# Performance work log

Hardware: AMD Instinct MI355X
Metric: run time of the kernel (lower is better)

The kernel has to match this reference:

```python
import jax, jax.numpy as jnp
import numpy as np

CLUSTER_DIM = 64
SHRINKAGE = True
EPS = 1e-8


def setup_inputs() -> dict:
    key = jax.random.key(0)
    x = jax.random.normal(key, (256, CLUSTER_DIM, 4096), dtype=jnp.float32)
    return {"x": x}


def _mat_shrinkage(C, n):
    # Rao-Blackwellized Ledoit-Wolf shrinkage toward scaled identity.
    p = CLUSTER_DIM
    I = jnp.eye(p, dtype=C.dtype)[None, :, :]
    trace = jnp.trace(C, axis1=-2, axis2=-1)[:, None, None]          # [B,1,1]
    F_hat = trace / p * I
    second_trace = jnp.einsum('bij,bji->b', C, C)[:, None, None]      # tr(C @ C)
    numerator = (n - 2) / n * second_trace + trace ** 2
    denominator = (n + 2) * (second_trace - trace ** 2 / p)
    rho = jnp.minimum(numerator / denominator, 1.0)
    return rho * F_hat + (1.0 - rho) * C


def reference(x):
    B, C, M = x.shape  # C == CLUSTER_DIM
    x_mu = jnp.mean(x, axis=2, keepdims=True)
    x_cnt = x - x_mu                                                  # [B,C,M]
    cov = jnp.einsum('bcm,bdm->bcd', x_cnt, x_cnt) / M                # [B,C,C]
    if SHRINKAGE:
        cov = _mat_shrinkage(cov, n=M)
    L, Q = jnp.linalg.eigh(cov)                                       # L:[B,C] Q:[B,C,C]
    L = jnp.maximum(L, EPS)
    # S_hat = Q @ diag(L^-1/2) @ Q^T, fused as scaled columns of Q
    S_hat = jnp.einsum('bik,bk,bjk->bij', Q, jax.lax.rsqrt(L), Q)     # [B,C,C]
    Z = jnp.einsum('bij,bjm->bim', S_hat, x_cnt)                      # [B,C,M]
    return Z
```

## Files before the change

### kernel.cpp

```cpp
#include <hip/hip_runtime.h>
#include <hip/hip_bf16.h>

#define BB 256
#define P 64
#define MM 4096
#define MC 128
#define MT 256

using bf16x8 = __attribute__((ext_vector_type(8))) short;
using f32x16 = __attribute__((ext_vector_type(16))) float;
using f32x4  = __attribute__((ext_vector_type(4))) float;
using u32x4  = __attribute__((ext_vector_type(4))) unsigned;
using u32x2  = __attribute__((ext_vector_type(2))) unsigned;

__device__ inline f32x16 MF(bf16x8 a, bf16x8 b, f32x16 c) {
    return __builtin_amdgcn_mfma_f32_32x32x16_bf16(a, b, c, 0, 0, 0);
}
__device__ inline unsigned cvtpk(float lo, float hi) {
    unsigned u;
    asm("v_cvt_pk_bf16_f32 %0, %1, %2" : "=v"(u) : "v"(lo), "v"(hi));
    return u;
}

template<bool XPK>
__global__ __launch_bounds__(256)
void covpart_kernel(const float* __restrict__ x, float* __restrict__ s2p,
                    float* __restrict__ s1p, unsigned* __restrict__ xpk, int nsplit)
{
    __shared__ __align__(16) unsigned char smem[34816];

    const int b = blockIdx.x, sp = blockIdx.y;
    const int t = threadIdx.x;
    const int w = t >> 6, l = t & 63;
    const int lr = l & 31, lh = l >> 5;
    const int mlen = MM / nsplit;
    const float* xb = x + (size_t)b * (P * MM) + (size_t)sp * mlen;
    unsigned* xpb = XPK ? (xpk + (size_t)b * (32 * MM) + (size_t)sp * mlen) : nullptr;

    f32x16 acc0 = {0,0,0,0,0,0,0,0,0,0,0,0,0,0,0,0};
    f32x16 acc1 = {0,0,0,0,0,0,0,0,0,0,0,0,0,0,0,0};
    f32x16 acc2 = {0,0,0,0,0,0,0,0,0,0,0,0,0,0,0,0};
    float s1e[4] = {0.f,0.f,0.f,0.f};
    float s1o[4] = {0.f,0.f,0.f,0.f};

    const int kbase = lh * 16;
    const int nch = mlen / MC;

    f32x4 ve[4], vo[4];
    #pragma unroll
    for (int j = 0; j < 4; ++j) {
        int slot = t + 256 * j;
        int dp = slot >> 5, c = (slot & 31) << 2;
        const float* p = xb + (size_t)(2 * dp) * MM + c;
        ve[j] = *reinterpret_cast<const f32x4*>(p);
        vo[j] = *reinterpret_cast<const f32x4*>(p + MM);
    }

    for (int ch = 0; ch < nch; ++ch) {
        char* buf = (char*)smem + (ch & 1) * 17408;
        #pragma unroll
        for (int j = 0; j < 4; ++j) {
            int slot = t + 256 * j;
            int dp = slot >> 5, c4 = slot & 31;
            float e0 = ve[j].x, e1 = ve[j].y, e2 = ve[j].z, e3 = ve[j].w;
            float o0 = vo[j].x, o1 = vo[j].y, o2 = vo[j].z, o3 = vo[j].w;
            s1e[j] += (e0 + e1) + (e2 + e3);
            s1o[j] += (o0 + o1) + (o2 + o3);
            u32x2 he, ho;
            he.x = cvtpk(e0, e1); he.y = cvtpk(e2, e3);
            ho.x = cvtpk(o0, o1); ho.y = cvtpk(o2, o3);
            char* dst = buf + (2 * dp) * 272 + c4 * 8;
            *reinterpret_cast<u32x2*>(dst) = he;
            *reinterpret_cast<u32x2*>(dst + 272) = ho;
            if (XPK) {
                u32x4 pd;
                pd.x = cvtpk(e0, o0); pd.y = cvtpk(e1, o1);
                pd.z = cvtpk(e2, o2); pd.w = cvtpk(e3, o3);
                *reinterpret_cast<u32x4*>(xpb + (size_t)dp * MM + ch * MC + c4 * 4) = pd;
            }
        }
        if (ch + 1 < nch) {
            const int m0 = (ch + 1) * MC;
            #pragma unroll
            for (int j = 0; j < 4; ++j) {
                int slot = t + 256 * j;
                int dp = slot >> 5, c = (slot & 31) << 2;
                const float* p = xb + (size_t)(2 * dp) * MM + m0 + c;
                ve[j] = *reinterpret_cast<const f32x4*>(p);
                vo[j] = *reinterpret_cast<const f32x4*>(p + MM);
            }
        }
        __syncthreads();
        #pragma unroll
        for (int kk = 0; kk < 2; ++kk) {
            const int kb = (2 * w + kk) * 32 + kbase;
            bf16x8 f0 = *(const bf16x8*)(buf + lr * 272 + kb);
            bf16x8 f1 = *(const bf16x8*)(buf + (32 + lr) * 272 + kb);
            acc0 = MF(f0, f0, acc0);
            acc1 = MF(f0, f1, acc1);
            acc2 = MF(f1, f1, acc2);
        }
    }

    float (*T)[32][33] = reinterpret_cast<float (*)[32][33]>(smem);
    float* s2b = s2p + ((size_t)sp * BB + b) * (P * P);

#define REDUCE_PASS(ACC, STORE)                                       \
    {                                                                 \
        __syncthreads();                                              \
        _Pragma("unroll")                                             \
        for (int n = 0; n < 16; ++n) {                                \
            int row = (n & 3) + 8 * (n >> 2) + 4 * lh;                \
            T[w][row][lr] = ACC[n];                                   \
        }                                                             \
        __syncthreads();                                              \
        _Pragma("unroll")                                             \
        for (int q = 0; q < 4; ++q) {                                 \
            int idx = t + 256 * q;                                    \
            int r = idx >> 5, c = idx & 31;                           \
            float s = T[0][r][c] + T[1][r][c] + T[2][r][c] + T[3][r][c]; \
            STORE                                                     \
        }                                                             \
    }

    REDUCE_PASS(acc0, s2b[r * 64 + c] = s;)
    REDUCE_PASS(acc1, s2b[r * 64 + 32 + c] = s; s2b[(32 + c) * 64 + r] = s;)
    REDUCE_PASS(acc2, s2b[(32 + r) * 64 + 32 + c] = s;)
#undef REDUCE_PASS

    #pragma unroll
    for (int m = 16; m >= 1; m >>= 1) {
        #pragma unroll
        for (int j = 0; j < 4; ++j) {
            s1e[j] += __shfl_xor(s1e[j], m);
            s1o[j] += __shfl_xor(s1o[j], m);
        }
    }
    if ((t & 31) == 0) {
        float* s1b = s1p + ((size_t)sp * BB + b) * P;
        int g = t >> 5;
        #pragma unroll
        for (int j = 0; j < 4; ++j) {
            int r0 = 2 * (g + 8 * j);
            s1b[r0]     = s1e[j];
            s1b[r0 + 1] = s1o[j];
        }
    }
}

typedef float (*Mat68)[68];

__device__ inline void mm64f(Mat68 D, Mat68 A, Mat68 Bm, int t, float alpha, float beta)
{
    __syncthreads();
    const int r0 = (t >> 4) * 4, c0 = (t & 15) * 4;
    float acc[4][4];
    #pragma unroll
    for (int i = 0; i < 4; ++i)
        #pragma unroll
        for (int j = 0; j < 4; ++j) acc[i][j] = 0.f;
    #pragma unroll 4
    for (int k = 0; k < P; ++k) {
        float av[4], bv[4];
        *reinterpret_cast<float4*>(av) = *reinterpret_cast<const float4*>(&A[k][r0]);
        *reinterpret_cast<float4*>(bv) = *reinterpret_cast<const float4*>(&Bm[k][c0]);
        #pragma unroll
        for (int i = 0; i < 4; ++i)
            #pragma unroll
            for (int j = 0; j < 4; ++j) acc[i][j] += av[i] * bv[j];
    }
    __syncthreads();
    #pragma unroll
    for (int i = 0; i < 4; ++i)
        #pragma unroll
        for (int j = 0; j < 4; ++j)
            D[r0 + i][c0 + j] = alpha * acc[i][j] + ((r0 + i) == (c0 + j) ? beta : 0.f);
}

__global__ __launch_bounds__(256)
void whiten_kernel(const float* __restrict__ s2p, const float* __restrict__ s1p,
                   unsigned* __restrict__ sbb, float* __restrict__ tvec, int nsplit)
{
    __shared__ __align__(16) float B0[P][68], B1[P][68], B2[P][68], B3[P][68], B4[P][68];
    __shared__ float mus[P];
    __shared__ float red[2][4];
    const int b = blockIdx.x, t = threadIdx.x;

    if (t < P) {
        float s = 0.f;
        for (int sp = 0; sp < nsplit; ++sp) s += s1p[((size_t)sp * BB + b) * P + t];
        mus[t] = s * (1.0f / MM);
    }
    __syncthreads();

    float tr_part = 0.f, s2_part = 0.f;
    #pragma unroll
    for (int j = 0; j < 16; ++j) {
        int f = t + 256 * j;
        int i = f >> 6, jc = f & 63;
        float sum = 0.f;
        for (int sp = 0; sp < nsplit; ++sp)
            sum += s2p[((size_t)sp * BB + b) * (P * P) + f];
        float v = sum * (1.0f / MM) - mus[i] * mus[jc];
        B0[i][jc] = v;
        s2_part += v * v;
        if (i == jc) tr_part += v;
    }
    #pragma unroll
    for (int off = 32; off > 0; off >>= 1) {
        tr_part += __shfl_down(tr_part, off);
        s2_part += __shfl_down(s2_part, off);
    }
    if ((t & 63) == 0) { red[0][t >> 6] = tr_part; red[1][t >> 6] = s2_part; }
    __syncthreads();
    const float trace = red[0][0] + red[0][1] + red[0][2] + red[0][3];
    const float sum2  = red[1][0] + red[1][1] + red[1][2] + red[1][3];

    const float nf = (float)MM;
    const float num = (nf - 2.0f) / nf * sum2 + trace * trace;
    const float den = (nf + 2.0f) * (sum2 - trace * trace / (float)P);
    const float rho = (den > 0.f) ? fminf(num / den, 1.0f) : 1.0f;
    const float lam = trace * (1.0f / P);
    const float inv_s = 1.0f / lam;

    #pragma unroll
    for (int j = 0; j < 16; ++j) {
        int f = t + 256 * j;
        int i = f >> 6, jc = f & 63;
        float v = B0[i][jc];
        float sv = ((1.0f - rho) * v + ((i == jc) ? rho * lam : 0.f)) * inv_s;
        B0[i][jc] = sv;
        B2[i][jc] = ((i == jc) ? 1.5f : 0.f) - 0.5f * sv;
    }

    mm64f(B1, B0, B2, t, 1.f, 0.f);
    Mat68 Yc = B1, Zc = B2, Tc = B0, U = B3, V = B4;
    {
        mm64f(Tc, Zc, Yc, t, -0.5f, 1.5f);
        mm64f(U,  Yc, Tc, t, 1.f, 0.f);
        mm64f(V,  Tc, Zc, t, 1.f, 0.f);
        Mat68 tmp = Yc; Yc = U; U = tmp;
        tmp = Zc; Zc = V; V = tmp;
    }
    mm64f(Tc, Zc, Yc, t, -0.5f, 1.5f);
    mm64f(U,  Tc, Zc, t, 1.f, 0.f);
    __syncthreads();

    const float sc = rsqrtf(lam);
    unsigned* sb = sbb + (size_t)b * (P * P / 2);
    #pragma unroll
    for (int j = 0; j < 8; ++j) {
        int slot = t + 256 * j;
        int dp = slot >> 6, row = slot & 63;
        sb[slot] = cvtpk(U[row][2 * dp] * sc, U[row][2 * dp + 1] * sc);
    }
    if (t < P) {
        float tv = 0.f;
        #pragma unroll
        for (int d = 0; d < P; ++d) tv += U[t][d] * mus[d];
        tvec[b * P + t] = tv * sc;
    }
}

__global__ __launch_bounds__(256)
void apply_kernel_x(const unsigned* __restrict__ xpk, const unsigned* __restrict__ sbb,
                    const float* __restrict__ tvec, float* __restrict__ out)
{
    __shared__ unsigned Spk[32][68];
    __shared__ unsigned Xpk[32][260];
    __shared__ float tvs[P];
    const int mt = blockIdx.x, b = blockIdx.y;
    const int t = threadIdx.x;
    const int w = t >> 6, l = t & 63;
    const int lr = l & 31, lh = l >> 5;

    const unsigned* sb = sbb + (size_t)b * (P * P / 2);
    #pragma unroll
    for (int j = 0; j < 8; ++j) {
        int slot = t + 256 * j;
        Spk[slot >> 6][slot & 63] = sb[slot];
    }
    if (t < P) tvs[t] = tvec[b * P + t];

    const unsigned* xb = xpk + (size_t)b * (32 * MM) + mt * MT;
    #pragma unroll
    for (int j = 0; j < 8; ++j) {
        int slot = t + 256 * j;
        int dp = slot >> 6, m0 = (slot & 63) * 4;
        u32x4 pk = *reinterpret_cast<const u32x4*>(xb + (size_t)dp * MM + m0);
        *reinterpret_cast<u32x4*>(&Xpk[dp][m0]) = pk;
    }
    __syncthreads();

    union U8 { unsigned u[4]; bf16x8 v; };
    bf16x8 sa0[4], sa1[4];
    #pragma unroll
    for (int ks = 0; ks < 4; ++ks) {
        const int dpb = ks * 8 + lh * 4;
        U8 x0, x1;
        #pragma unroll
        for (int q = 0; q < 4; ++q) {
            x0.u[q] = Spk[dpb + q][lr];
            x1.u[q] = Spk[dpb + q][32 + lr];
        }
        sa0[ks] = x0.v;
        sa1[ks] = x1.v;
    }

    f32x16 acc00 = {0,0,0,0,0,0,0,0,0,0,0,0,0,0,0,0};
    f32x16 acc01 = {0,0,0,0,0,0,0,0,0,0,0,0,0,0,0,0};
    f32x16 acc10 = {0,0,0,0,0,0,0,0,0,0,0,0,0,0,0,0};
    f32x16 acc11 = {0,0,0,0,0,0,0,0,0,0,0,0,0,0,0,0};

    const int cq0 = (2 * w) * 32 + lr, cq1 = cq0 + 32;
    #pragma unroll
    for (int ks = 0; ks < 4; ++ks) {
        const int dpb = ks * 8 + lh * 4;
        U8 b0, b1;
        #pragma unroll
        for (int q = 0; q < 4; ++q) {
            b0.u[q] = Xpk[dpb + q][cq0];
            b1.u[q] = Xpk[dpb + q][cq1];
        }
        acc00 = MF(sa0[ks], b0.v, acc00);
        acc01 = MF(sa0[ks], b1.v, acc01);
        acc10 = MF(sa1[ks], b0.v, acc10);
        acc11 = MF(sa1[ks], b1.v, acc11);
    }

    float* ob = out + (size_t)b * (P * MM) + mt * MT;
#define STORE_TILE(ACC, RT, CQ)                                          \
    {                                                                    \
        _Pragma("unroll")                                                \
        for (int n = 0; n < 16; ++n) {                                   \
            int row = (RT) * 32 + (n & 3) + 8 * (n >> 2) + 4 * lh;       \
            __builtin_nontemporal_store(ACC[n] - tvs[row],               \
                                        ob + (size_t)row * MM + (CQ));   \
        }                                                                \
    }
    STORE_TILE(acc00, 0, cq0)
    STORE_TILE(acc01, 0, cq1)
    STORE_TILE(acc10, 1, cq0)
    STORE_TILE(acc11, 1, cq1)
#undef STORE_TILE
}

__global__ __launch_bounds__(256)
void apply_kernel(const float* __restrict__ x, const unsigned* __restrict__ sbb,
                  const float* __restrict__ tvec, float* __restrict__ out)
{
    __shared__ unsigned Spk[32][68];
    __shared__ unsigned Xpk[32][260];
    __shared__ float tvs[P];
    const int mt = blockIdx.x, b = blockIdx.y;
    const int t = threadIdx.x;
    const int w = t >> 6, l = t & 63;
    const int lr = l & 31, lh = l >> 5;

    const unsigned* sb = sbb + (size_t)b * (P * P / 2);
    #pragma unroll
    for (int j = 0; j < 8; ++j) {
        int slot = t + 256 * j;
        Spk[slot >> 6][slot & 63] = sb[slot];
    }
    if (t < P) tvs[t] = tvec[b * P + t];

    const float* xb = x + (size_t)b * (P * MM) + mt * MT;
    #pragma unroll
    for (int j = 0; j < 8; ++j) {
        int slot = t + 256 * j;
        int dp = slot >> 6, m0 = (slot & 63) * 4;
        const float* xr = xb + (size_t)(2 * dp) * MM + m0;
        f32x4 a = *reinterpret_cast<const f32x4*>(xr);
        f32x4 c = *reinterpret_cast<const f32x4*>(xr + MM);
        uint4 pk = make_uint4(cvtpk(a.x, c.x), cvtpk(a.y, c.y),
                              cvtpk(a.z, c.z), cvtpk(a.w, c.w));
        *reinterpret_cast<uint4*>(&Xpk[dp][m0]) = pk;
    }
    __syncthreads();

    union U8 { unsigned u[4]; bf16x8 v; };
    bf16x8 sa0[4], sa1[4];
    #pragma unroll
    for (int ks = 0; ks < 4; ++ks) {
        const int dpb = ks * 8 + lh * 4;
        U8 x0, x1;
        #pragma unroll
        for (int q = 0; q < 4; ++q) {
            x0.u[q] = Spk[dpb + q][lr];
            x1.u[q] = Spk[dpb + q][32 + lr];
        }
        sa0[ks] = x0.v;
        sa1[ks] = x1.v;
    }

    f32x16 acc00 = {0,0,0,0,0,0,0,0,0,0,0,0,0,0,0,0};
    f32x16 acc01 = {0,0,0,0,0,0,0,0,0,0,0,0,0,0,0,0};
    f32x16 acc10 = {0,0,0,0,0,0,0,0,0,0,0,0,0,0,0,0};
    f32x16 acc11 = {0,0,0,0,0,0,0,0,0,0,0,0,0,0,0,0};

    const int cq0 = (2 * w) * 32 + lr, cq1 = cq0 + 32;
    #pragma unroll
    for (int ks = 0; ks < 4; ++ks) {
        const int dpb = ks * 8 + lh * 4;
        U8 b0, b1;
        #pragma unroll
        for (int q = 0; q < 4; ++q) {
            b0.u[q] = Xpk[dpb + q][cq0];
            b1.u[q] = Xpk[dpb + q][cq1];
        }
        acc00 = MF(sa0[ks], b0.v, acc00);
        acc01 = MF(sa0[ks], b1.v, acc01);
        acc10 = MF(sa1[ks], b0.v, acc10);
        acc11 = MF(sa1[ks], b1.v, acc11);
    }

    float* ob = out + (size_t)b * (P * MM) + mt * MT;
#define STORE_TILE(ACC, RT, CQ)                                          \
    {                                                                    \
        _Pragma("unroll")                                                \
        for (int n = 0; n < 16; ++n) {                                   \
            int row = (RT) * 32 + (n & 3) + 8 * (n >> 2) + 4 * lh;       \
            __builtin_nontemporal_store(ACC[n] - tvs[row],               \
                                        ob + (size_t)row * MM + (CQ));   \
        }                                                                \
    }
    STORE_TILE(acc00, 0, cq0)
    STORE_TILE(acc01, 0, cq1)
    STORE_TILE(acc10, 1, cq0)
    STORE_TILE(acc11, 1, cq1)
#undef STORE_TILE
}

extern "C" void kernel_launch(void* const* d_in, const int* in_sizes, int n_in,
                              void* d_out, int out_size, void* d_ws, size_t ws_size,
                              hipStream_t stream)
{
    const float* x = (const float*)d_in[0];
    float* out = (float*)d_out;

    auto need = [](int ns) -> size_t {
        return ((size_t)ns * BB * P * P + (size_t)ns * BB * P
                + (size_t)BB * P * P / 2 + (size_t)BB * P) * sizeof(float);
    };
    const size_t xpk_bytes = (size_t)BB * 32 * MM * sizeof(unsigned);

    int nsplit;
    bool xon;
    if (ws_size >= need(4) + xpk_bytes)      { nsplit = 4; xon = true; }
    else if (ws_size >= need(2) + xpk_bytes) { nsplit = 2; xon = true; }
    else {
        xon = false;
        nsplit = (ws_size >= need(4)) ? 4 : (ws_size >= need(2)) ? 2 : 1;
    }

    float* s2p  = (float*)d_ws;
    float* s1p  = s2p + (size_t)nsplit * BB * P * P;
    unsigned* sbb = (unsigned*)(s1p + (size_t)nsplit * BB * P);
    float* tvec = (float*)(sbb + (size_t)BB * P * P / 2);
    unsigned* xpk = (unsigned*)(tvec + (size_t)BB * P);

    if (xon) {
        covpart_kernel<true><<<dim3(BB, nsplit), 256, 0, stream>>>(x, s2p, s1p, xpk, nsplit);
        whiten_kernel<<<dim3(BB), 256, 0, stream>>>(s2p, s1p, sbb, tvec, nsplit);
        apply_kernel_x<<<dim3(MM / MT, BB), 256, 0, stream>>>(xpk, sbb, tvec, out);
    } else {
        covpart_kernel<false><<<dim3(BB, nsplit), 256, 0, stream>>>(x, s2p, s1p, nullptr, nsplit);
        whiten_kernel<<<dim3(BB), 256, 0, stream>>>(s2p, s1p, sbb, tvec, nsplit);
        apply_kernel<<<dim3(MM / MT, BB), 256, 0, stream>>>(x, sbb, tvec, out);
    }
}
```

Baseline: 187.0 us.

## Halve covariance chunk width, prefetch two chunks ahead, raise split count

The covariance-partial kernel now processes 64-column chunks instead of 128, keeps two register buffers, and prefetches two chunks ahead, so more global loads are in flight per thread. Shared memory per block drops, which can allow more resident blocks. The host also tries an 8-way M split to launch more blocks. In exchange there are more partial covariance matrices for the whiten kernel to reduce and more loop iterations with a barrier each. The fallback path no longer allows nsplit=1, so it requires more workspace.

```diff
diff --git a/kernel.cpp b/kernel.cpp
--- a/kernel.cpp
+++ b/kernel.cpp
@@ -4,7 +4,8 @@
 #define BB 256
 #define P 64
 #define MM 4096
-#define MC 128
+#define MCC 64
+#define RSB 144
 #define MT 256
 
 using bf16x8 = __attribute__((ext_vector_type(8))) short;
@@ -27,7 +28,7 @@
 void covpart_kernel(const float* __restrict__ x, float* __restrict__ s2p,
                     float* __restrict__ s1p, unsigned* __restrict__ xpk, int nsplit)
 {
-    __shared__ __align__(16) unsigned char smem[34816];
+    __shared__ __align__(16) unsigned char smem[2 * 64 * RSB];
 
     const int b = blockIdx.x, sp = blockIdx.y;
     const int t = threadIdx.x;
@@ -40,66 +41,66 @@
     f32x16 acc0 = {0,0,0,0,0,0,0,0,0,0,0,0,0,0,0,0};
     f32x16 acc1 = {0,0,0,0,0,0,0,0,0,0,0,0,0,0,0,0};
     f32x16 acc2 = {0,0,0,0,0,0,0,0,0,0,0,0,0,0,0,0};
-    float s1e[4] = {0.f,0.f,0.f,0.f};
-    float s1o[4] = {0.f,0.f,0.f,0.f};
-
-    const int kbase = lh * 16;
-    const int nch = mlen / MC;
-
-    f32x4 ve[4], vo[4];
-    #pragma unroll
-    for (int j = 0; j < 4; ++j) {
-        int slot = t + 256 * j;
-        int dp = slot >> 5, c = (slot & 31) << 2;
-        const float* p = xb + (size_t)(2 * dp) * MM + c;
-        ve[j] = *reinterpret_cast<const f32x4*>(p);
-        vo[j] = *reinterpret_cast<const f32x4*>(p + MM);
+    float s1e[2] = {0.f, 0.f};
+    float s1o[2] = {0.f, 0.f};
+
+    const int kboff = w * 32 + lh * 16;
+    const int nch = mlen / MCC;
+
+    f32x4 vA[2][2], vB[2][2];
+    #pragma unroll
+    for (int j = 0; j < 2; ++j) {
+        int slot = t + 256 * j;
+        int pr = slot >> 4, c = (slot & 15) << 2;
+        const float* p = xb + (size_t)(2 * pr) * MM + c;
+        vA[j][0] = *reinterpret_cast<const f32x4*>(p);
+        vA[j][1] = *reinterpret_cast<const f32x4*>(p + MM);
+        const float* p1 = p + MCC;
+        vB[j][0] = *reinterpret_cast<const f32x4*>(p1);
+        vB[j][1] = *reinterpret_cast<const f32x4*>(p1 + MM);
     }
 
     for (int ch = 0; ch < nch; ++ch) {
-        char* buf = (char*)smem + (ch & 1) * 17408;
-        #pragma unroll
-        for (int j = 0; j < 4; ++j) {
+        char* buf = (char*)smem + (ch & 1) * (64 * RSB);
+        f32x4 (*vc)[2] = (ch & 1) ? vB : vA;
+        #pragma unroll
+        for (int j = 0; j < 2; ++j) {
             int slot = t + 256 * j;
-            int dp = slot >> 5, c4 = slot & 31;
-            float e0 = ve[j].x, e1 = ve[j].y, e2 = ve[j].z, e3 = ve[j].w;
-            float o0 = vo[j].x, o1 = vo[j].y, o2 = vo[j].z, o3 = vo[j].w;
+            int pr = slot >> 4, c4 = slot & 15;
+            float e0 = vc[j][0].x, e1 = vc[j][0].y, e2 = vc[j][0].z, e3 = vc[j][0].w;
+            float o0 = vc[j][1].x, o1 = vc[j][1].y, o2 = vc[j][1].z, o3 = vc[j][1].w;
             s1e[j] += (e0 + e1) + (e2 + e3);
             s1o[j] += (o0 + o1) + (o2 + o3);
             u32x2 he, ho;
             he.x = cvtpk(e0, e1); he.y = cvtpk(e2, e3);
             ho.x = cvtpk(o0, o1); ho.y = cvtpk(o2, o3);
-            char* dst = buf + (2 * dp) * 272 + c4 * 8;
+            char* dst = buf + (2 * pr) * RSB + c4 * 8;
             *reinterpret_cast<u32x2*>(dst) = he;
-            *reinterpret_cast<u32x2*>(dst + 272) = ho;
+            *reinterpret_cast<u32x2*>(dst + RSB) = ho;
             if (XPK) {
                 u32x4 pd;
                 pd.x = cvtpk(e0, o0); pd.y = cvtpk(e1, o1);
                 pd.z = cvtpk(e2, o2); pd.w = cvtpk(e3, o3);
-                *reinterpret_cast<u32x4*>(xpb + (size_t)dp * MM + ch * MC + c4 * 4) = pd;
+                *reinterpret_cast<u32x4*>(xpb + (size_t)pr * MM + ch * MCC + c4 * 4) = pd;
             }
         }
-        if (ch + 1 < nch) {
-            const int m0 = (ch + 1) * MC;
+        if (ch + 2 < nch) {
+            const int m0 = (ch + 2) * MCC;
             #pragma unroll
-            for (int j = 0; j < 4; ++j) {
+            for (int j = 0; j < 2; ++j) {
                 int slot = t + 256 * j;
-                int dp = slot >> 5, c = (slot & 31) << 2;
-                const float* p = xb + (size_t)(2 * dp) * MM + m0 + c;
-                ve[j] = *reinterpret_cast<const f32x4*>(p);
-                vo[j] = *reinterpret_cast<const f32x4*>(p + MM);
+                int pr = slot >> 4, c = (slot & 15) << 2;
+                const float* p = xb + (size_t)(2 * pr) * MM + m0 + c;
+                vc[j][0] = *reinterpret_cast<const f32x4*>(p);
+                vc[j][1] = *reinterpret_cast<const f32x4*>(p + MM);
             }
         }
         __syncthreads();
-        #pragma unroll
-        for (int kk = 0; kk < 2; ++kk) {
-            const int kb = (2 * w + kk) * 32 + kbase;
-            bf16x8 f0 = *(const bf16x8*)(buf + lr * 272 + kb);
-            bf16x8 f1 = *(const bf16x8*)(buf + (32 + lr) * 272 + kb);
-            acc0 = MF(f0, f0, acc0);
-            acc1 = MF(f0, f1, acc1);
-            acc2 = MF(f1, f1, acc2);
-        }
+        bf16x8 f0 = *(const bf16x8*)(buf + lr * RSB + kboff);
+        bf16x8 f1 = *(const bf16x8*)(buf + (32 + lr) * RSB + kboff);
+        acc0 = MF(f0, f0, acc0);
+        acc1 = MF(f0, f1, acc1);
+        acc2 = MF(f1, f1, acc2);
     }
 
     float (*T)[32][33] = reinterpret_cast<float (*)[32][33]>(smem);
@@ -129,21 +130,21 @@
 #undef REDUCE_PASS
 
     #pragma unroll
-    for (int m = 16; m >= 1; m >>= 1) {
-        #pragma unroll
-        for (int j = 0; j < 4; ++j) {
+    for (int m = 8; m >= 1; m >>= 1) {
+        #pragma unroll
+        for (int j = 0; j < 2; ++j) {
             s1e[j] += __shfl_xor(s1e[j], m);
             s1o[j] += __shfl_xor(s1o[j], m);
         }
     }
-    if ((t & 31) == 0) {
+    if ((l & 15) == 0) {
         float* s1b = s1p + ((size_t)sp * BB + b) * P;
-        int g = t >> 5;
-        #pragma unroll
-        for (int j = 0; j < 4; ++j) {
-            int r0 = 2 * (g + 8 * j);
-            s1b[r0]     = s1e[j];
-            s1b[r0 + 1] = s1o[j];
+        int pbase = w * 4 + (l >> 4);
+        #pragma unroll
+        for (int j = 0; j < 2; ++j) {
+            int pr = pbase + 16 * j;
+            s1b[2 * pr]     = s1e[j];
+            s1b[2 * pr + 1] = s1o[j];
         }
     }
 }
@@ -447,11 +448,12 @@
 
     int nsplit;
     bool xon;
-    if (ws_size >= need(4) + xpk_bytes)      { nsplit = 4; xon = true; }
+    if (ws_size >= need(8) + xpk_bytes)      { nsplit = 8; xon = true; }
+    else if (ws_size >= need(4) + xpk_bytes) { nsplit = 4; xon = true; }
     else if (ws_size >= need(2) + xpk_bytes) { nsplit = 2; xon = true; }
     else {
         xon = false;
-        nsplit = (ws_size >= need(4)) ? 4 : (ws_size >= need(2)) ? 2 : 1;
+        nsplit = (ws_size >= need(8)) ? 8 : (ws_size >= need(4)) ? 4 : 2;
     }
 
     float* s2p  = (float*)d_ws;
```

After: 216.4 us. +15.8%, slower.
